# Optimization experiments

Measured on AMD Instinct MI355X. Metric: run time of the kernel, lower is better.

The kernel has to match this reference:

```python
import jax, jax.numpy as jnp
import numpy as np

B, CIN, COUT, H, W, K = 4, 3, 16, 256, 256, 5
PAD = K // 2  # replicate padding keeps spatial size


def _dilation_sum(x, w):
    """Learnable dilation, channel_merge_mode='sum'.
    x: (B,Cin,H,W), w: (Cout,Cin,K,K).
    out[b,o,i,j] = sum_c max_{di,dj} ( x_pad[b,c,i+di,j+dj] + w[o,c,di,dj] )
    """
    xp = jnp.pad(x, ((0, 0), (0, 0), (PAD, PAD), (PAD, PAD)), mode='edge')
    acc = jnp.full((x.shape[0], w.shape[0], x.shape[1], H, W), -jnp.inf, dtype=x.dtype)
    for di in range(K):  # fixed small kernel loop (unrolled), not a data-dim loop
        for dj in range(K):
            win = xp[:, :, di:di + H, dj:dj + W]                     # (B,Cin,H,W)
            cand = win[:, None] + w[None, :, :, di, dj][:, :, :, None, None]  # (B,Cout,Cin,H,W)
            acc = jnp.maximum(acc, cand)
    return acc.sum(axis=2)  # merge over input channels -> (B,Cout,H,W)


def _erosion_identity(y, w):
    """Learnable erosion, channel_merge_mode='identity' (each channel independent).
    y: (B,Cout,H,W), w: (Cout,K,K).
    out[b,o,i,j] = min_{di,dj} ( y_pad[b,o,i+di,j+dj] - w[o,di,dj] )
    """
    yp = jnp.pad(y, ((0, 0), (0, 0), (PAD, PAD), (PAD, PAD)), mode='edge')
    acc = jnp.full(y.shape, jnp.inf, dtype=y.dtype)
    for di in range(K):
        for dj in range(K):
            acc = jnp.minimum(acc, yp[:, :, di:di + H, dj:dj + W] - w[None, :, di, dj, None, None])
    return acc


def setup_inputs() -> dict:
    key = jax.random.key(0)
    k1, k2, k3 = jax.random.split(key, 3)
    x = jax.random.normal(k1, (B, CIN, H, W), dtype=jnp.float32)
    w_d = jax.random.normal(k2, (COUT, CIN, K, K), dtype=jnp.float32) * 0.05
    w_e = jax.random.normal(k3, (COUT, K, K), dtype=jnp.float32) * 0.05
    return {"x": x, "w_d": w_d, "w_e": w_e}


def reference(x, w_d, w_e):
    # Closing = dilation (max-plus, sum merge) followed by erosion (min-plus, identity merge)
    dilated = _dilation_sum(x, w_d)
    return _erosion_identity(dilated, w_e)
```

## Files before the change

### kernel.cpp

```cpp
#include <hip/hip_runtime.h>
#include <float.h>


namespace {
constexpr int HH = 256, WW = 256, CI = 3;
constexpr int TT = 32;
constexpr int DS = 44;
constexpr int XS = 44;
constexpr int XR = 40;
constexpr int XCH = XR * XS;
}

__device__ __forceinline__ float4 dapp(float4 m, float4 A, float4 B,
                                       float w0, float w1, float w2, float w3, float w4) {
    m.x = fmaxf(fmaxf(fmaxf(m.x, A.x + w0), fmaxf(A.y + w1, A.z + w2)), fmaxf(A.w + w3, B.x + w4));
    m.y = fmaxf(fmaxf(fmaxf(m.y, A.y + w0), fmaxf(A.z + w1, A.w + w2)), fmaxf(B.x + w3, B.y + w4));
    m.z = fmaxf(fmaxf(fmaxf(m.z, A.z + w0), fmaxf(A.w + w1, B.x + w2)), fmaxf(B.y + w3, B.z + w4));
    m.w = fmaxf(fmaxf(fmaxf(m.w, A.w + w0), fmaxf(B.x + w1, B.y + w2)), fmaxf(B.z + w3, B.w + w4));
    return m;
}

__device__ __forceinline__ void add4(float4& a, float4 m) {
    a.x += m.x; a.y += m.y; a.z += m.z; a.w += m.w;
}

__global__ __launch_bounds__(256, 4)
void closing_v3(const float* __restrict__ x, const float* __restrict__ wd,
                const float* __restrict__ we, float* __restrict__ out) {
    __shared__ __align__(16) float sx[CI * XCH];
    __shared__ __align__(16) float sdil[36 * DS];

    const int tid = threadIdx.x;
    const int bx = blockIdx.x, by = blockIdx.y, z = blockIdx.z;
    const int o = z & 15, b = z >> 4;
    const int i0 = by * TT, j0 = bx * TT;
    const float* xb = x + (size_t)b * (CI * HH * WW);

#pragma unroll
    for (int k = 0; k < 19; ++k) {
        const int idx = tid + (k << 8);
        if (idx < CI * XR * XR) {
            const int c   = idx / 1600;
            const int rem = idx - c * 1600;
            const int rr  = rem / 40;
            const int cc  = rem - rr * 40;
            int gi = i0 - 4 + rr; gi = min(max(gi, 0), HH - 1);
            int gj = j0 - 4 + cc; gj = min(max(gj, 0), WW - 1);
            sx[c * XCH + rr * XS + cc] = xb[c * (HH * WW) + (gi << 8) + gj];
        }
    }
    __syncthreads();

    if (tid < 81) {
        const int q = tid / 9, s = tid - q * 9;
        float4 acc0 = {0,0,0,0}, acc1 = acc0, acc2 = acc0, acc3 = acc0;
#pragma unroll
        for (int c = 0; c < CI; ++c) {
            const float* wr = wd + (o * CI + c) * 25;
            const float* base = &sx[c * XCH + (4 * q) * XS + 4 * s];
            const float NEG = -FLT_MAX;
            float4 m0 = {NEG,NEG,NEG,NEG}, m1 = m0, m2 = m0, m3 = m0;
#pragma unroll
            for (int dd = 0; dd < 8; ++dd) {
                const float4 A = *(const float4*)(base + dd * XS);
                const float4 B = *(const float4*)(base + dd * XS + 4);
                if (dd <= 4)           m0 = dapp(m0, A, B, wr[dd*5+0], wr[dd*5+1], wr[dd*5+2], wr[dd*5+3], wr[dd*5+4]);
                if (dd >= 1 && dd <= 5){ const int k2 = dd-1;
                                       m1 = dapp(m1, A, B, wr[k2*5+0], wr[k2*5+1], wr[k2*5+2], wr[k2*5+3], wr[k2*5+4]); }
                if (dd >= 2 && dd <= 6){ const int k2 = dd-2;
                                       m2 = dapp(m2, A, B, wr[k2*5+0], wr[k2*5+1], wr[k2*5+2], wr[k2*5+3], wr[k2*5+4]); }
                if (dd >= 3)           { const int k2 = dd-3;
                                       m3 = dapp(m3, A, B, wr[k2*5+0], wr[k2*5+1], wr[k2*5+2], wr[k2*5+3], wr[k2*5+4]); }
            }
            add4(acc0, m0); add4(acc1, m1); add4(acc2, m2); add4(acc3, m3);
        }

        if (bx == 0 && s == 0) {
            acc0.x = acc0.y = acc0.z;  acc1.x = acc1.y = acc1.z;
            acc2.x = acc2.y = acc2.z;  acc3.x = acc3.y = acc3.z;
        }
        if (bx == 7 && s == 8) {
            acc0.z = acc0.w = acc0.y;  acc1.z = acc1.w = acc1.y;
            acc2.z = acc2.w = acc2.y;  acc3.z = acc3.w = acc3.y;
        }
        float4 w0 = acc0, w1 = acc1, w2 = acc2, w3 = acc3;
        if (by == 0 && q == 0) { w0 = acc2; w1 = acc2; }
        if (by == 7 && q == 8) { w2 = acc1; w3 = acc1; }
        float* dp = &sdil[(4 * q) * DS + 4 * s];
        *(float4*)(dp)          = w0;
        *(float4*)(dp + DS)     = w1;
        *(float4*)(dp + 2 * DS) = w2;
        *(float4*)(dp + 3 * DS) = w3;
    }
    __syncthreads();

    if (tid < 128) {
        const int s = tid & 3, r = tid >> 2;
        const float* ew = we + o * 25;
        const float* eb = &sdil[r * DS + 8 * s];
        const float PF = FLT_MAX;
        float4 r0 = {PF,PF,PF,PF}, r1 = r0;
#pragma unroll
        for (int dd = 0; dd < 5; ++dd) {
            const float4 A = *(const float4*)(eb + dd * DS);
            const float4 B = *(const float4*)(eb + dd * DS + 4);
            const float4 C = *(const float4*)(eb + dd * DS + 8);
            const float e0 = ew[dd*5+0], e1 = ew[dd*5+1], e2 = ew[dd*5+2],
                        e3 = ew[dd*5+3], e4 = ew[dd*5+4];
            r0.x = fminf(fminf(fminf(r0.x, A.x - e0), fminf(A.y - e1, A.z - e2)), fminf(A.w - e3, B.x - e4));
            r0.y = fminf(fminf(fminf(r0.y, A.y - e0), fminf(A.z - e1, A.w - e2)), fminf(B.x - e3, B.y - e4));
            r0.z = fminf(fminf(fminf(r0.z, A.z - e0), fminf(A.w - e1, B.x - e2)), fminf(B.y - e3, B.z - e4));
            r0.w = fminf(fminf(fminf(r0.w, A.w - e0), fminf(B.x - e1, B.y - e2)), fminf(B.z - e3, B.w - e4));
            r1.x = fminf(fminf(fminf(r1.x, B.x - e0), fminf(B.y - e1, B.z - e2)), fminf(B.w - e3, C.x - e4));
            r1.y = fminf(fminf(fminf(r1.y, B.y - e0), fminf(B.z - e1, B.w - e2)), fminf(C.x - e3, C.y - e4));
            r1.z = fminf(fminf(fminf(r1.z, B.z - e0), fminf(B.w - e1, C.x - e2)), fminf(C.y - e3, C.z - e4));
            r1.w = fminf(fminf(fminf(r1.w, B.w - e0), fminf(C.x - e1, C.y - e2)), fminf(C.z - e3, C.w - e4));
        }
        float* op = &out[((size_t)z << 16) + ((size_t)(i0 + r) << 8) + j0 + 8 * s];
        *(float4*)op       = r0;
        *(float4*)(op + 4) = r1;
    }
}

extern "C" void kernel_launch(void* const* d_in, const int* in_sizes, int n_in,
                              void* d_out, int out_size, void* d_ws, size_t ws_size,
                              hipStream_t stream) {
    const float* x  = (const float*)d_in[0];
    const float* wd = (const float*)d_in[1];
    const float* we = (const float*)d_in[2];
    float* out = (float*)d_out;

    dim3 grid(WW / TT, HH / TT, 4 * 16);
    closing_v3<<<grid, dim3(256), 0, stream>>>(x, wd, we, out);
}
```

Measured before the change: 110.1 us.

## Enlarge tiles to 64x56, vectorize interior loads, use all threads

Grows each block's output tile from 32x32 to 64 wide by 56 tall. This gives a 4x5 grid per channel image, with the last row-tile overlapping the previous one, and cuts the cost of recomputing halo rows in the dilation stage. Interior column tiles load the input with float4 global reads, while edge tiles keep scalar clamped loads. Dilation now uses 255 threads instead of 81 and the erosion loop covers all threads, so far fewer threads sit idle. The max/min trees are reordered into chains. The trade-offs are more shared memory, lower occupancy (launch bounds 2), and some redundant work in the overlapping last row tile.

```diff
diff --git a/kernel.cpp b/kernel.cpp
--- a/kernel.cpp
+++ b/kernel.cpp
@@ -4,19 +4,26 @@
 
 namespace {
 constexpr int HH = 256, WW = 256, CI = 3;
-constexpr int TT = 32;
-constexpr int DS = 44;
-constexpr int XS = 44;
-constexpr int XR = 40;
-constexpr int XCH = XR * XS;
+constexpr int TW = 64, TH = 56;
+constexpr int DS = 68;
+constexpr int XS = 76;
+constexpr int XCH = 64 * XS;
 }
 
 __device__ __forceinline__ float4 dapp(float4 m, float4 A, float4 B,
                                        float w0, float w1, float w2, float w3, float w4) {
-    m.x = fmaxf(fmaxf(fmaxf(m.x, A.x + w0), fmaxf(A.y + w1, A.z + w2)), fmaxf(A.w + w3, B.x + w4));
-    m.y = fmaxf(fmaxf(fmaxf(m.y, A.y + w0), fmaxf(A.z + w1, A.w + w2)), fmaxf(B.x + w3, B.y + w4));
-    m.z = fmaxf(fmaxf(fmaxf(m.z, A.z + w0), fmaxf(A.w + w1, B.x + w2)), fmaxf(B.y + w3, B.z + w4));
-    m.w = fmaxf(fmaxf(fmaxf(m.w, A.w + w0), fmaxf(B.x + w1, B.y + w2)), fmaxf(B.z + w3, B.w + w4));
+    {   float u = fmaxf(fmaxf(A.x + w0, A.y + w1), A.z + w2);
+        float v = fmaxf(fmaxf(u, A.w + w3), B.x + w4);
+        m.x = fmaxf(m.x, v); }
+    {   float u = fmaxf(fmaxf(A.y + w0, A.z + w1), A.w + w2);
+        float v = fmaxf(fmaxf(u, B.x + w3), B.y + w4);
+        m.y = fmaxf(m.y, v); }
+    {   float u = fmaxf(fmaxf(A.z + w0, A.w + w1), B.x + w2);
+        float v = fmaxf(fmaxf(u, B.y + w3), B.z + w4);
+        m.z = fmaxf(m.z, v); }
+    {   float u = fmaxf(fmaxf(A.w + w0, B.x + w1), B.y + w2);
+        float v = fmaxf(fmaxf(u, B.z + w3), B.w + w4);
+        m.w = fmaxf(m.w, v); }
     return m;
 }
 
@@ -24,35 +31,50 @@
     a.x += m.x; a.y += m.y; a.z += m.z; a.w += m.w;
 }
 
-__global__ __launch_bounds__(256, 4)
-void closing_v3(const float* __restrict__ x, const float* __restrict__ wd,
+__global__ __launch_bounds__(256, 2)
+void closing_v4(const float* __restrict__ x, const float* __restrict__ wd,
                 const float* __restrict__ we, float* __restrict__ out) {
     __shared__ __align__(16) float sx[CI * XCH];
-    __shared__ __align__(16) float sdil[36 * DS];
+    __shared__ __align__(16) float sdil[60 * DS];
 
     const int tid = threadIdx.x;
     const int bx = blockIdx.x, by = blockIdx.y, z = blockIdx.z;
     const int o = z & 15, b = z >> 4;
-    const int i0 = by * TT, j0 = bx * TT;
+    const int i0 = min(by * TH, HH - TH);
+    const int j0 = bx * TW;
     const float* xb = x + (size_t)b * (CI * HH * WW);
 
+    const bool colsafe = (bx != 0) && (bx != 3);
+    if (colsafe) {
 #pragma unroll
-    for (int k = 0; k < 19; ++k) {
-        const int idx = tid + (k << 8);
-        if (idx < CI * XR * XR) {
-            const int c   = idx / 1600;
-            const int rem = idx - c * 1600;
-            const int rr  = rem / 40;
-            const int cc  = rem - rr * 40;
-            int gi = i0 - 4 + rr; gi = min(max(gi, 0), HH - 1);
-            int gj = j0 - 4 + cc; gj = min(max(gj, 0), WW - 1);
-            sx[c * XCH + rr * XS + cc] = xb[c * (HH * WW) + (gi << 8) + gj];
+        for (int k = 0; k < 14; ++k) {
+            const int idx = tid + (k << 8);
+            if (idx < 3456) {
+                const int c   = idx / 1152;
+                const int rem = idx - c * 1152;
+                const int r   = rem / 18;
+                const int cq  = rem - r * 18;
+                int gi = i0 - 4 + r; gi = min(max(gi, 0), HH - 1);
+                const float4 v = *(const float4*)&xb[c * (HH*WW) + (gi << 8) + (j0 - 4) + (cq << 2)];
+                *(float4*)&sx[c * XCH + r * XS + (cq << 2)] = v;
+            }
+        }
+    } else {
+        for (int k = 0; k < 54; ++k) {
+            const int idx = tid + (k << 8);
+            const int c   = idx / 4608;
+            const int rem = idx - c * 4608;
+            const int r   = rem / 72;
+            const int col = rem - r * 72;
+            int gi = i0 - 4 + r;   gi = min(max(gi, 0), HH - 1);
+            int gj = j0 - 4 + col; gj = min(max(gj, 0), WW - 1);
+            sx[c * XCH + r * XS + col] = xb[c * (HH*WW) + (gi << 8) + gj];
         }
     }
     __syncthreads();
 
-    if (tid < 81) {
-        const int q = tid / 9, s = tid - q * 9;
+    if (tid < 255) {
+        const int q = tid / 17, s = tid - q * 17;
         float4 acc0 = {0,0,0,0}, acc1 = acc0, acc2 = acc0, acc3 = acc0;
 #pragma unroll
         for (int c = 0; c < CI; ++c) {
@@ -64,13 +86,13 @@
             for (int dd = 0; dd < 8; ++dd) {
                 const float4 A = *(const float4*)(base + dd * XS);
                 const float4 B = *(const float4*)(base + dd * XS + 4);
-                if (dd <= 4)           m0 = dapp(m0, A, B, wr[dd*5+0], wr[dd*5+1], wr[dd*5+2], wr[dd*5+3], wr[dd*5+4]);
-                if (dd >= 1 && dd <= 5){ const int k2 = dd-1;
-                                       m1 = dapp(m1, A, B, wr[k2*5+0], wr[k2*5+1], wr[k2*5+2], wr[k2*5+3], wr[k2*5+4]); }
-                if (dd >= 2 && dd <= 6){ const int k2 = dd-2;
-                                       m2 = dapp(m2, A, B, wr[k2*5+0], wr[k2*5+1], wr[k2*5+2], wr[k2*5+3], wr[k2*5+4]); }
-                if (dd >= 3)           { const int k2 = dd-3;
-                                       m3 = dapp(m3, A, B, wr[k2*5+0], wr[k2*5+1], wr[k2*5+2], wr[k2*5+3], wr[k2*5+4]); }
+                if (dd <= 4)            m0 = dapp(m0, A, B, wr[dd*5+0], wr[dd*5+1], wr[dd*5+2], wr[dd*5+3], wr[dd*5+4]);
+                if (dd >= 1 && dd <= 5) { const int k2 = dd-1;
+                                        m1 = dapp(m1, A, B, wr[k2*5+0], wr[k2*5+1], wr[k2*5+2], wr[k2*5+3], wr[k2*5+4]); }
+                if (dd >= 2 && dd <= 6) { const int k2 = dd-2;
+                                        m2 = dapp(m2, A, B, wr[k2*5+0], wr[k2*5+1], wr[k2*5+2], wr[k2*5+3], wr[k2*5+4]); }
+                if (dd >= 3)            { const int k2 = dd-3;
+                                        m3 = dapp(m3, A, B, wr[k2*5+0], wr[k2*5+1], wr[k2*5+2], wr[k2*5+3], wr[k2*5+4]); }
             }
             add4(acc0, m0); add4(acc1, m1); add4(acc2, m2); add4(acc3, m3);
         }
@@ -79,13 +101,13 @@
             acc0.x = acc0.y = acc0.z;  acc1.x = acc1.y = acc1.z;
             acc2.x = acc2.y = acc2.z;  acc3.x = acc3.y = acc3.z;
         }
-        if (bx == 7 && s == 8) {
+        if (bx == 3 && s == 16) {
             acc0.z = acc0.w = acc0.y;  acc1.z = acc1.w = acc1.y;
             acc2.z = acc2.w = acc2.y;  acc3.z = acc3.w = acc3.y;
         }
         float4 w0 = acc0, w1 = acc1, w2 = acc2, w3 = acc3;
-        if (by == 0 && q == 0) { w0 = acc2; w1 = acc2; }
-        if (by == 7 && q == 8) { w2 = acc1; w3 = acc1; }
+        if (i0 == 0        && q == 0)  { w0 = acc2; w1 = acc2; }
+        if (i0 == HH - TH  && q == 14) { w2 = acc1; w3 = acc1; }
         float* dp = &sdil[(4 * q) * DS + 4 * s];
         *(float4*)(dp)          = w0;
         *(float4*)(dp + DS)     = w1;
@@ -94,31 +116,49 @@
     }
     __syncthreads();
 
-    if (tid < 128) {
-        const int s = tid & 3, r = tid >> 2;
+    {
         const float* ew = we + o * 25;
-        const float* eb = &sdil[r * DS + 8 * s];
-        const float PF = FLT_MAX;
-        float4 r0 = {PF,PF,PF,PF}, r1 = r0;
+        for (int t = tid; t < 448; t += 256) {
+            const int r = t >> 3, s = t & 7;
+            const float* eb = &sdil[r * DS + 8 * s];
+            const float PF = FLT_MAX;
+            float4 r0 = {PF,PF,PF,PF}, r1 = r0;
 #pragma unroll
-        for (int dd = 0; dd < 5; ++dd) {
-            const float4 A = *(const float4*)(eb + dd * DS);
-            const float4 B = *(const float4*)(eb + dd * DS + 4);
-            const float4 C = *(const float4*)(eb + dd * DS + 8);
-            const float e0 = ew[dd*5+0], e1 = ew[dd*5+1], e2 = ew[dd*5+2],
-                        e3 = ew[dd*5+3], e4 = ew[dd*5+4];
-            r0.x = fminf(fminf(fminf(r0.x, A.x - e0), fminf(A.y - e1, A.z - e2)), fminf(A.w - e3, B.x - e4));
-            r0.y = fminf(fminf(fminf(r0.y, A.y - e0), fminf(A.z - e1, A.w - e2)), fminf(B.x - e3, B.y - e4));
-            r0.z = fminf(fminf(fminf(r0.z, A.z - e0), fminf(A.w - e1, B.x - e2)), fminf(B.y - e3, B.z - e4));
-            r0.w = fminf(fminf(fminf(r0.w, A.w - e0), fminf(B.x - e1, B.y - e2)), fminf(B.z - e3, B.w - e4));
-            r1.x = fminf(fminf(fminf(r1.x, B.x - e0), fminf(B.y - e1, B.z - e2)), fminf(B.w - e3, C.x - e4));
-            r1.y = fminf(fminf(fminf(r1.y, B.y - e0), fminf(B.z - e1, B.w - e2)), fminf(C.x - e3, C.y - e4));
-            r1.z = fminf(fminf(fminf(r1.z, B.z - e0), fminf(B.w - e1, C.x - e2)), fminf(C.y - e3, C.z - e4));
-            r1.w = fminf(fminf(fminf(r1.w, B.w - e0), fminf(C.x - e1, C.y - e2)), fminf(C.z - e3, C.w - e4));
+            for (int dd = 0; dd < 5; ++dd) {
+                const float4 A = *(const float4*)(eb + dd * DS);
+                const float4 B = *(const float4*)(eb + dd * DS + 4);
+                const float4 C = *(const float4*)(eb + dd * DS + 8);
+                const float e0 = ew[dd*5+0], e1 = ew[dd*5+1], e2 = ew[dd*5+2],
+                            e3 = ew[dd*5+3], e4 = ew[dd*5+4];
+                {   float u = fminf(fminf(A.x - e0, A.y - e1), A.z - e2);
+                    float v = fminf(fminf(u, A.w - e3), B.x - e4);
+                    r0.x = fminf(r0.x, v); }
+                {   float u = fminf(fminf(A.y - e0, A.z - e1), A.w - e2);
+                    float v = fminf(fminf(u, B.x - e3), B.y - e4);
+                    r0.y = fminf(r0.y, v); }
+                {   float u = fminf(fminf(A.z - e0, A.w - e1), B.x - e2);
+                    float v = fminf(fminf(u, B.y - e3), B.z - e4);
+                    r0.z = fminf(r0.z, v); }
+                {   float u = fminf(fminf(A.w - e0, B.x - e1), B.y - e2);
+                    float v = fminf(fminf(u, B.z - e3), B.w - e4);
+                    r0.w = fminf(r0.w, v); }
+                {   float u = fminf(fminf(B.x - e0, B.y - e1), B.z - e2);
+                    float v = fminf(fminf(u, B.w - e3), C.x - e4);
+                    r1.x = fminf(r1.x, v); }
+                {   float u = fminf(fminf(B.y - e0, B.z - e1), B.w - e2);
+                    float v = fminf(fminf(u, C.x - e3), C.y - e4);
+                    r1.y = fminf(r1.y, v); }
+                {   float u = fminf(fminf(B.z - e0, B.w - e1), C.x - e2);
+                    float v = fminf(fminf(u, C.y - e3), C.z - e4);
+                    r1.z = fminf(r1.z, v); }
+                {   float u = fminf(fminf(B.w - e0, C.x - e1), C.y - e2);
+                    float v = fminf(fminf(u, C.z - e3), C.w - e4);
+                    r1.w = fminf(r1.w, v); }
+            }
+            float* op = &out[((size_t)z << 16) + ((size_t)(i0 + r) << 8) + j0 + 8 * s];
+            *(float4*)op       = r0;
+            *(float4*)(op + 4) = r1;
         }
-        float* op = &out[((size_t)z << 16) + ((size_t)(i0 + r) << 8) + j0 + 8 * s];
-        *(float4*)op       = r0;
-        *(float4*)(op + 4) = r1;
     }
 }
 
@@ -130,6 +170,6 @@
     const float* we = (const float*)d_in[2];
     float* out = (float*)d_out;
 
-    dim3 grid(WW / TT, HH / TT, 4 * 16);
-    closing_v3<<<grid, dim3(256), 0, stream>>>(x, wd, we, out);
+    dim3 grid(WW / TW, 5, 4 * 16);
+    closing_v4<<<grid, dim3(256), 0, stream>>>(x, wd, we, out);
 }
```

New measurement: 108.0 us. Within noise of the previous version (-1.9%).
